# Kernel tuning notes

Measured on AMD Instinct MI355X. Metric: run time of the kernel, lower is better.

The kernel has to match this reference:

```python
import jax, jax.numpy as jnp
import numpy as np

NUM_CLASSES = 10
CLS_W, L1_W, GIOU_W = 2.0, 5.0, 2.0


def box_cxcywh_to_xyxy(b):
    cx, cy, w, h = b[..., 0], b[..., 1], b[..., 2], b[..., 3]
    return jnp.stack([cx - w / 2, cy - h / 2, cx + w / 2, cy + h / 2], axis=-1)


def giou_matrix(b1, b2):
    # b1: (B,N,4), b2: (B,M,4) xyxy -> (B,N,M)
    a1 = jnp.clip(b1[..., 2] - b1[..., 0], 0) * jnp.clip(b1[..., 3] - b1[..., 1], 0)
    a2 = jnp.clip(b2[..., 2] - b2[..., 0], 0) * jnp.clip(b2[..., 3] - b2[..., 1], 0)
    lt = jnp.maximum(b1[..., :, None, :2], b2[..., None, :, :2])
    rb = jnp.minimum(b1[..., :, None, 2:], b2[..., None, :, 2:])
    wh = jnp.clip(rb - lt, 0)
    inter = wh[..., 0] * wh[..., 1]
    union = a1[..., :, None] + a2[..., None, :] - inter
    iou = inter / jnp.clip(union, 1e-6)
    lte = jnp.minimum(b1[..., :, None, :2], b2[..., None, :, :2])
    rbe = jnp.maximum(b1[..., :, None, 2:], b2[..., None, :, 2:])
    whe = jnp.clip(rbe - lte, 0)
    enc = whe[..., 0] * whe[..., 1]
    return iou - (enc - union) / jnp.clip(enc, 1e-6)


def giou_elem(b1, b2):
    # b1, b2: (N,4) xyxy, paired -> (N,)
    a1 = jnp.clip(b1[:, 2] - b1[:, 0], 0) * jnp.clip(b1[:, 3] - b1[:, 1], 0)
    a2 = jnp.clip(b2[:, 2] - b2[:, 0], 0) * jnp.clip(b2[:, 3] - b2[:, 1], 0)
    lt = jnp.maximum(b1[:, :2], b2[:, :2])
    rb = jnp.minimum(b1[:, 2:], b2[:, 2:])
    wh = jnp.clip(rb - lt, 0)
    inter = wh[:, 0] * wh[:, 1]
    union = a1 + a2 - inter
    iou = inter / jnp.clip(union, 1e-6)
    lte = jnp.minimum(b1[:, :2], b2[:, :2])
    rbe = jnp.maximum(b1[:, 2:], b2[:, 2:])
    whe = jnp.clip(rbe - lte, 0)
    enc = whe[:, 0] * whe[:, 1]
    return iou - (enc - union) / jnp.clip(enc, 1e-6)


def hungarian(cost):
    # Jonker-Volgenant style shortest-augmenting-path assignment (== scipy.linear_sum_assignment)
    cost = np.asarray(cost, dtype=np.float64)
    transposed = cost.shape[0] > cost.shape[1]
    C = cost.T if transposed else cost
    n, m = C.shape  # n <= m
    u = np.zeros(n + 1)
    v = np.zeros(m + 1)
    p = np.zeros(m + 1, dtype=np.int64)
    colr = np.arange(m + 1)
    for i in range(1, n + 1):
        p[0] = i
        j0 = 0
        minv = np.full(m + 1, np.inf)
        way = np.zeros(m + 1, dtype=np.int64)
        used = np.zeros(m + 1, dtype=bool)
        while True:
            used[j0] = True
            i0 = p[j0]
            unused = colr[1:][~used[1:]]
            cur = C[i0 - 1, unused - 1] - u[i0] - v[unused]
            better = cur < minv[unused]
            bidx = unused[better]
            minv[bidx] = cur[better]
            way[bidx] = j0
            j1 = unused[np.argmin(minv[unused])]
            delta = minv[j1]
            u[p[used]] += delta
            v[used] -= delta
            minv[~used] -= delta
            j0 = j1
            if p[j0] == 0:
                break
        while j0 != 0:
            jn = way[j0]
            p[j0] = p[jn]
            j0 = jn
    rows = p[1:] - 1
    cols = np.arange(m)
    sel = rows >= 0
    r, c = rows[sel], cols[sel]
    if transposed:
        r, c = c, r
    order = np.argsort(r)
    return r[order], c[order]


def compute_matches(pred_logits, pred_boxes, gt_classes, gt_boxes):
    # Batched cost matrices on device, per-sample Hungarian on host (mirrors torch.no_grad matcher).
    B, Q, _ = pred_logits.shape
    G = gt_classes.shape[1]
    prob = jax.nn.softmax(pred_logits, axis=-1)
    cls_idx = jnp.clip(gt_classes, 0, NUM_CLASSES - 1)
    idx = jnp.broadcast_to(cls_idx[:, None, :], (B, Q, G))
    cls_cost = -jnp.take_along_axis(prob, idx, axis=2)                 # (B,Q,G)
    l1_cost = jnp.abs(pred_boxes[:, :, None, :] - gt_boxes[:, None, :, :]).sum(-1)
    g = giou_matrix(box_cxcywh_to_xyxy(pred_boxes), box_cxcywh_to_xyxy(gt_boxes))
    cost = CLS_W * cls_cost + L1_W * l1_cost - GIOU_W * g
    cost_np = np.asarray(jax.device_get(cost))
    valid_np = np.asarray(jax.device_get(gt_classes)) >= 0
    bs, ps, gs = [], [], []
    for bi in range(B):
        vidx = np.nonzero(valid_np[bi])[0]
        if vidx.size == 0:
            continue
        r, c = hungarian(cost_np[bi][:, vidx])
        bs.append(np.full(r.size, bi, dtype=np.int64))
        ps.append(r.astype(np.int64))
        gs.append(vidx[c].astype(np.int64))
    if bs:
        return np.concatenate(bs), np.concatenate(ps), np.concatenate(gs)
    z = np.zeros(0, np.int64)
    return z, z, z


def detection_loss(pred_logits, pred_boxes, gt_boxes, target_cls, b_f, p_f, g_f, n_matched):
    C1 = pred_logits.shape[-1]
    logp = jax.nn.log_softmax(pred_logits, axis=-1).reshape(-1, C1)
    t = target_cls.reshape(-1)
    w = jnp.ones(C1, dtype=pred_logits.dtype).at[-1].set(0.1)
    nll = -jnp.take_along_axis(logp, t[:, None], axis=1)[:, 0]
    wt = w[t]
    cls_loss = (wt * nll).sum() / wt.sum()
    mp = pred_boxes[b_f, p_f]
    mg = gt_boxes[b_f, g_f]
    l1 = jnp.abs(mp - mg).sum()
    gd = giou_elem(box_cxcywh_to_xyxy(mp), box_cxcywh_to_xyxy(mg))
    gl = (1.0 - gd).sum()
    return CLS_W * cls_loss + L1_W * l1 / n_matched + GIOU_W * gl / n_matched


def setup_inputs() -> dict:
    key = jax.random.key(0)
    k1, k2, k3, k4, k5 = jax.random.split(key, 5)
    B, Q, G, C = 64, 900, 100, NUM_CLASSES
    pred_logits = jax.random.normal(k1, (B, Q, C + 1), dtype=jnp.float32)
    pred_boxes = jax.random.uniform(k2, (B, Q, 4), dtype=jnp.float32, minval=0.05, maxval=0.6)
    gt_boxes = jax.random.uniform(k3, (B, G, 4), dtype=jnp.float32, minval=0.05, maxval=0.6)
    cls = jax.random.randint(k4, (B, G), 0, C)
    nvalid = jax.random.randint(k5, (B,), 1, G + 1)
    mask = jnp.arange(G)[None, :] < nvalid[:, None]
    gt_classes = jnp.where(mask, cls, -1).astype(jnp.int32)
    return {"pred_logits": pred_logits, "pred_boxes": pred_boxes,
            "gt_classes": gt_classes, "gt_boxes": gt_boxes}


def reference(pred_logits, pred_boxes, gt_classes, gt_boxes):
    B, Q = pred_logits.shape[:2]
    b_f, p_f, g_f = compute_matches(pred_logits, pred_boxes, gt_classes, gt_boxes)
    gt_np = np.asarray(jax.device_get(gt_classes))
    tc = np.full((B, Q), NUM_CLASSES, dtype=np.int32)
    tc[b_f, p_f] = gt_np[b_f, g_f]
    n_matched = max(int(b_f.size), 1)
    return detection_loss(pred_logits, pred_boxes, gt_boxes, jnp.asarray(tc), b_f, p_f, g_f, n_matched)
```

## Files before the change

### kernel.cpp

```cpp
#include <hip/hip_runtime.h>
#include <hip/hip_bf16.h>
#include <math.h>

#define BB 64
#define QQ 900
#define GG 100
#define NCLS 10
#define CP1 11

#define STRIDE 960
#define KPL 15
#define NT 512
#define NW 8
#define QMASK 255
#define ROUND_CAP 20000

#define NCH 8
#define QCH 128

#define CLS_W 2.0f
#define L1_W 5.0f
#define GIOU_W 2.0f

struct Accum {
  double wnll, wt, l1, gl;
  int nm, counter;
  int pad[6];
};

__global__ __launch_bounds__(256) void cost_kernel(
    const float* __restrict__ logits, const float* __restrict__ pboxes,
    const int* __restrict__ gcls, const float* __restrict__ gboxes,
    float* __restrict__ cost, float4* __restrict__ part, Accum* acc) {
  const int b = blockIdx.y;
  const int chunk = blockIdx.x;
  const int tid = threadIdx.x;
  const int ql = tid & (QCH - 1);
  const int gh = tid >> 7;
  const int q = chunk * QCH + ql;

  if (chunk == 0 && b == 0 && tid == 0) {
    acc->wnll = 0.0; acc->wt = 0.0; acc->l1 = 0.0; acc->gl = 0.0;
    acc->nm = 0; acc->counter = 0;
  }

  __shared__ float s_gb[GG * 4];
  __shared__ int   s_gc[GG];
  __shared__ float s_prob[QCH * 13];
  __shared__ float s_c[GG][QCH + 1];
  __shared__ float pm1[2][GG], pm2[2][GG];
  __shared__ int   pj1[2][GG];
  __shared__ int   sh_n;

  if (tid == 0) sh_n = 0;
  __syncthreads();

  for (int i = tid; i < GG * 4; i += 256) s_gb[i] = gboxes[b * GG * 4 + i];
  for (int i = tid; i < GG; i += 256) {
    const int v = gcls[b * GG + i];
    s_gc[i] = v;
    if (v >= 0) atomicAdd(&sh_n, 1);
  }

  float pcx = 0.f, pcy = 0.f, pw = 0.f, ph = 0.f;
  if (q < QQ) {
    const float* pb = pboxes + ((size_t)b * QQ + q) * 4;
    pcx = pb[0]; pcy = pb[1]; pw = pb[2]; ph = pb[3];
    if (gh == 0) {
      const float* lg = logits + ((size_t)b * QQ + q) * CP1;
      float l[CP1];
      float mx = -1e30f;
      for (int c = 0; c < CP1; ++c) { l[c] = lg[c]; mx = fmaxf(mx, l[c]); }
      float se = 0.f;
      for (int c = 0; c < CP1; ++c) { l[c] = expf(l[c] - mx); se += l[c]; }
      const float inv = 1.0f / se;
      for (int c = 0; c < NCLS; ++c) s_prob[ql * 13 + c] = l[c] * inv;
    }
  }
  __syncthreads();
  const int sn = sh_n;

  const float px1 = pcx - 0.5f * pw, py1 = pcy - 0.5f * ph;
  const float px2 = pcx + 0.5f * pw, py2 = pcy + 0.5f * ph;
  const float pa = fmaxf(px2 - px1, 0.f) * fmaxf(py2 - py1, 0.f);

  float* crow = cost + ((size_t)b * GG) * STRIDE + q;
  for (int g = gh; g < sn; g += 2) {
    float cv = 3e38f;
    if (q < QQ) {
      int cls = s_gc[g];
      cls = cls < 0 ? 0 : (cls > NCLS - 1 ? NCLS - 1 : cls);
      const float cc = -s_prob[ql * 13 + cls];
      const float gcx = s_gb[g * 4 + 0], gcy = s_gb[g * 4 + 1];
      const float gw  = s_gb[g * 4 + 2], gh2 = s_gb[g * 4 + 3];
      const float l1 = fabsf(pcx - gcx) + fabsf(pcy - gcy) + fabsf(pw - gw) + fabsf(ph - gh2);
      const float gx1 = gcx - 0.5f * gw, gy1 = gcy - 0.5f * gh2;
      const float gx2 = gcx + 0.5f * gw, gy2 = gcy + 0.5f * gh2;
      const float ga = fmaxf(gx2 - gx1, 0.f) * fmaxf(gy2 - gy1, 0.f);
      const float ltx = fmaxf(px1, gx1), lty = fmaxf(py1, gy1);
      const float rbx = fminf(px2, gx2), rby = fminf(py2, gy2);
      const float iw = fmaxf(rbx - ltx, 0.f), ih = fmaxf(rby - lty, 0.f);
      const float inter = iw * ih;
      const float uni = pa + ga - inter;
      const float iou = inter / fmaxf(uni, 1e-6f);
      const float ex1 = fminf(px1, gx1), ey1 = fminf(py1, gy1);
      const float ex2 = fmaxf(px2, gx2), ey2 = fmaxf(py2, gy2);
      const float ew = fmaxf(ex2 - ex1, 0.f), eh = fmaxf(ey2 - ey1, 0.f);
      const float enc = ew * eh;
      const float giou = iou - (enc - uni) / fmaxf(enc, 1e-6f);
      cv = CLS_W * cc + L1_W * l1 - GIOU_W * giou;
      crow[(size_t)g * STRIDE] = cv;
    } else if (q < STRIDE) {
      crow[(size_t)g * STRIDE] = 1e30f;
    }
    s_c[g][ql] = cv;
  }
  __syncthreads();

  {
    const int kmax = (chunk == NCH - 1) ? (QQ - (NCH - 1) * QCH) : QCH;
    const int half = tid >> 7;
    const int r = tid & 127;
    if (r < sn) {
      const int k0 = half ? 64 : 0;
      const int k1 = half ? kmax : (kmax < 64 ? kmax : 64);
      float m1 = 3e38f, m2 = 3e38f;
      int j1 = 0x7FFFFFFF;
      for (int k = k0; k < k1; ++k) {
        const float c = s_c[r][k];
        if (c < m1) { m2 = m1; m1 = c; j1 = 1 + chunk * QCH + k; }
        else if (c < m2) m2 = c;
      }
      pm1[half][r] = m1; pm2[half][r] = m2; pj1[half][r] = j1;
    }
    __syncthreads();
    if (tid < sn) {
      float m1 = pm1[0][tid], m2 = pm2[0][tid];
      int j1 = pj1[0][tid];
      const float n1 = pm1[1][tid], n2 = pm2[1][tid];
      const int i1 = pj1[1][tid];
      if (n1 < m1) { m2 = fminf(m1, n2); m1 = n1; j1 = i1; }
      else m2 = fminf(m2, n1);
      part[((size_t)b * NCH + chunk) * QCH + tid] = make_float4(m1, m2, __int_as_float(j1), 0.f);
    }
  }
}

__global__ __launch_bounds__(NT) void jv_kernel(
    const float* __restrict__ logits, const float* __restrict__ pboxes,
    const int* __restrict__ gcls, const float* __restrict__ gboxes,
    const float* __restrict__ cost, const float4* __restrict__ part,
    Accum* acc, float* out) {
  const int b = blockIdx.x;
  const int tid = threadIdx.x;
  const int lane = tid & 63;
  const int w = tid >> 6;

  __shared__ float vl[STRIDE + 2];
  __shared__ int   p[QQ + 1];
  __shared__ unsigned long long way64[STRIDE + 2];
  __shared__ float m1l[GG + 1], m2l[GG + 1];
  __shared__ int   aminl[GG + 1];
  __shared__ int   s_gc[GG];
  __shared__ int   queue[QMASK + 1];
  __shared__ int   sh_n, sh_qtail, sh_head;
  __shared__ double r0[NW], r1[NW], r2[NW], r3[NW];
  __shared__ int r4[NW];
  __shared__ float s_lse[QQ], s_mx[QQ];

  if (tid == 0) { sh_n = 0; sh_qtail = 0; sh_head = 0; }
  for (int j = tid; j <= QQ; j += NT) p[j] = 0;
  for (int j = tid; j < STRIDE + 2; j += NT) { vl[j] = 0.f; way64[j] = 0ull; }
  if (tid < GG) s_gc[tid] = gcls[b * GG + tid];
  __syncthreads();
  if (tid < GG && s_gc[tid] >= 0) atomicAdd(&sh_n, 1);
  __syncthreads();
  const int n = sh_n;
  const float* Cb = cost + (size_t)b * GG * STRIDE;

  for (int r = tid; r < n; r += NT) {
    float m1 = 3e38f, m2 = 3e38f;
    int j1 = 0x7FFFFFFF;
#pragma unroll
    for (int ch = 0; ch < NCH; ++ch) {
      const float4 pr = part[((size_t)b * NCH + ch) * QCH + r];
      const float pm1 = pr.x, pm2 = pr.y;
      if (pm1 < m1) { m2 = fminf(m1, pm2); m1 = pm1; j1 = __float_as_int(pr.z); }
      else m2 = fminf(m2, pm1);
    }
    m1l[r] = m1; m2l[r] = m2; aminl[r] = j1;
  }
  for (int qq = tid; qq < QQ; qq += NT) {
    const float* lg = logits + ((size_t)b * QQ + qq) * CP1;
    float l[CP1];
    float mx = -1e30f;
    for (int c = 0; c < CP1; ++c) { l[c] = lg[c]; mx = fmaxf(mx, l[c]); }
    float se = 0.f;
    for (int c = 0; c < CP1; ++c) se += expf(l[c] - mx);
    s_mx[qq] = mx;
    s_lse[qq] = logf(se);
  }
  __syncthreads();

  if (tid < n) {
    const float regret = m2l[tid] - m1l[tid];
    const unsigned long long key =
        ((unsigned long long)__float_as_uint(regret) << 20) | (unsigned long long)(tid + 1);
    atomicMax(&way64[aminl[tid]], key);
  }
  __syncthreads();
  if (tid < n) {
    const int j1 = aminl[tid];
    if ((int)(way64[j1] & 0xFFFFFu) == tid + 1) {
      p[j1] = tid + 1;
      vl[j1] = m1l[tid] - m2l[tid];
    } else {
      const int t0 = atomicAdd(&sh_qtail, 1);
      queue[t0 & QMASK] = tid + 1;
    }
  }
  __syncthreads();
  for (int j = tid; j < STRIDE + 2; j += NT) way64[j] = 0ull;
  __syncthreads();

  {
    float pfA[KPL], pfB[KPL];
    int pfAok = 0, pfBok = 0, pfArid = 0, pfBrid = 0;
    int kround = 0;
    while (kround < ROUND_CAP) {
      const int head = sh_head, tail = sh_qtail;
      const int nq = tail - head;
      if (nq <= 0) break;
      const int take = nq < 2 * NW ? nq : 2 * NW;
      ++kround;
      const bool doA = (2 * w < take);
      const bool doB = (2 * w + 1 < take);
      int ridA = 0, ridB = 0;
      float m1A = 3e38f, m2A = 3e38f, m1B = 3e38f, m2B = 3e38f;
      int j1A = 0x7FFFFFFF, j1B = 0x7FFFFFFF;
      if (doA) {
        float rcA[KPL], rcB[KPL];
        if (pfAok) { ridA = pfArid;
#pragma unroll
          for (int k = 0; k < KPL; ++k) rcA[k] = pfA[k];
        } else {
          ridA = queue[(head + 2 * w) & QMASK];
          const float* Cr = Cb + (size_t)(ridA - 1) * STRIDE + lane;
#pragma unroll
          for (int k = 0; k < KPL; ++k) rcA[k] = Cr[k << 6];
        }
        if (doB) {
          if (pfBok) { ridB = pfBrid;
#pragma unroll
            for (int k = 0; k < KPL; ++k) rcB[k] = pfB[k];
          } else {
            ridB = queue[(head + 2 * w + 1) & QMASK];
            const float* Cr = Cb + (size_t)(ridB - 1) * STRIDE + lane;
#pragma unroll
            for (int k = 0; k < KPL; ++k) rcB[k] = Cr[k << 6];
          }
        } else {
#pragma unroll
          for (int k = 0; k < KPL; ++k) rcB[k] = 3e38f;
        }
        float nA1 = 3e38f, nA2 = 3e38f, nB1 = 3e38f, nB2 = 3e38f;
        int iA1 = 0x7FFFFFFF, iB1 = 0x7FFFFFFF;
#pragma unroll
        for (int k = 0; k < 8; ++k) {
          const float vv = vl[1 + lane + (k << 6)];
          const float cA = rcA[k] - vv;
          if (cA < m1A) { m2A = m1A; m1A = cA; j1A = 1 + lane + (k << 6); }
          else if (cA < m2A) m2A = cA;
          const float cB = rcB[k] - vv;
          if (cB < m1B) { m2B = m1B; m1B = cB; j1B = 1 + lane + (k << 6); }
          else if (cB < m2B) m2B = cB;
        }
#pragma unroll
        for (int k = 8; k < KPL; ++k) {
          const float vv = vl[1 + lane + (k << 6)];
          const float cA = rcA[k] - vv;
          if (cA < nA1) { nA2 = nA1; nA1 = cA; iA1 = 1 + lane + (k << 6); }
          else if (cA < nA2) nA2 = cA;
          const float cB = rcB[k] - vv;
          if (cB < nB1) { nB2 = nB1; nB1 = cB; iB1 = 1 + lane + (k << 6); }
          else if (cB < nB2) nB2 = cB;
        }
        if (nA1 < m1A) { m2A = fminf(m1A, nA2); m1A = nA1; j1A = iA1; }
        else m2A = fminf(m2A, nA1);
        if (nB1 < m1B) { m2B = fminf(m1B, nB2); m1B = nB1; j1B = iB1; }
        else m2B = fminf(m2B, nB1);
        for (int m = 1; m < 64; m <<= 1) {
          const float oA1 = __shfl_xor(m1A, m), oA2 = __shfl_xor(m2A, m);
          const int ojA = __shfl_xor(j1A, m);
          const float oB1 = __shfl_xor(m1B, m), oB2 = __shfl_xor(m2B, m);
          const int ojB = __shfl_xor(j1B, m);
          if (oA1 < m1A) { m2A = fminf(m1A, oA2); m1A = oA1; j1A = ojA; }
          else m2A = fminf(m2A, oA1);
          if (oB1 < m1B) { m2B = fminf(m1B, oB2); m1B = oB1; j1B = ojB; }
          else m2B = fminf(m2B, oB1);
        }
        if (lane == 0) {
          float dA = m2A - m1A;
          if (dA < 0.f) dA = 0.f;
          const unsigned long long keyA = ((unsigned long long)kround << 44) |
              ((unsigned long long)__float_as_uint(dA) << 12) | (unsigned long long)ridA;
          atomicMax(&way64[j1A], keyA);
          if (doB) {
            float dB = m2B - m1B;
            if (dB < 0.f) dB = 0.f;
            const unsigned long long keyB = ((unsigned long long)kround << 44) |
                ((unsigned long long)__float_as_uint(dB) << 12) | (unsigned long long)ridB;
            atomicMax(&way64[j1B], keyB);
          }
        }
      }
      pfAok = 0; pfBok = 0;
      {
        const int nh = head + take;
        const int pA = nh + 2 * w, pB = pA + 1;
        if (pA < tail) {
          pfArid = queue[pA & QMASK];
          const float* Cr = Cb + (size_t)(pfArid - 1) * STRIDE + lane;
#pragma unroll
          for (int k = 0; k < KPL; ++k) pfA[k] = Cr[k << 6];
          pfAok = 1;
        }
        if (pB < tail) {
          pfBrid = queue[pB & QMASK];
          const float* Cr = Cb + (size_t)(pfBrid - 1) * STRIDE + lane;
#pragma unroll
          for (int k = 0; k < KPL; ++k) pfB[k] = Cr[k << 6];
          pfBok = 1;
        }
      }
      __syncthreads();
      if (lane == 0 && doA) {
        if ((int)(way64[j1A] & 0xFFFu) == ridA) {
          float dA = m2A - m1A;
          if (dA < 0.f) dA = 0.f;
          const float ov = vl[j1A];
          float nv = ov - dA;
          if (!(nv < ov)) nv = nextafterf(ov, -3e38f);
          vl[j1A] = nv;
          const int k0 = p[j1A];
          p[j1A] = ridA;
          if (k0 > 0) { const int t0 = atomicAdd(&sh_qtail, 1); queue[t0 & QMASK] = k0; }
        } else {
          const int t0 = atomicAdd(&sh_qtail, 1);
          queue[t0 & QMASK] = ridA;
        }
        if (doB) {
          if ((int)(way64[j1B] & 0xFFFu) == ridB) {
            float dB = m2B - m1B;
            if (dB < 0.f) dB = 0.f;
            const float ov = vl[j1B];
            float nv = ov - dB;
            if (!(nv < ov)) nv = nextafterf(ov, -3e38f);
            vl[j1B] = nv;
            const int k0 = p[j1B];
            p[j1B] = ridB;
            if (k0 > 0) { const int t0 = atomicAdd(&sh_qtail, 1); queue[t0 & QMASK] = k0; }
          } else {
            const int t0 = atomicAdd(&sh_qtail, 1);
            queue[t0 & QMASK] = ridB;
          }
        }
      }
      if (tid == 0) sh_head = head + take;
      __syncthreads();
    }
  }
  __syncthreads();

  double wnll = 0.0, wt = 0.0, l1d = 0.0, gld = 0.0;
  int nm = 0;
  for (int q = tid; q < QQ; q += NT) {
    const int idx = b * QQ + q;
    const int g = p[q + 1] - 1;
    const int t = (g >= 0) ? s_gc[g] : NCLS;
    const float lt = logits[(size_t)idx * CP1 + t];
    const float logp = (lt - s_mx[q]) - s_lse[q];
    const float wgt = (t == NCLS) ? 0.1f : 1.0f;
    wnll += (double)(wgt * (-logp));
    wt += (double)wgt;
    if (g >= 0) {
      nm += 1;
      const float* pb = pboxes + (size_t)idx * 4;
      const float* gb = gboxes + ((size_t)b * GG + g) * 4;
      const float pcx = pb[0], pcy = pb[1], pw = pb[2], ph = pb[3];
      const float gcx = gb[0], gcy = gb[1], gw = gb[2], gh = gb[3];
      const float l1 = fabsf(pcx - gcx) + fabsf(pcy - gcy) + fabsf(pw - gw) + fabsf(ph - gh);
      const float px1 = pcx - 0.5f * pw, py1 = pcy - 0.5f * ph;
      const float px2 = pcx + 0.5f * pw, py2 = pcy + 0.5f * ph;
      const float gx1 = gcx - 0.5f * gw, gy1 = gcy - 0.5f * gh;
      const float gx2 = gcx + 0.5f * gw, gy2 = gcy + 0.5f * gh;
      const float pa = fmaxf(px2 - px1, 0.f) * fmaxf(py2 - py1, 0.f);
      const float ga = fmaxf(gx2 - gx1, 0.f) * fmaxf(gy2 - gy1, 0.f);
      const float ltx = fmaxf(px1, gx1), lty = fmaxf(py1, gy1);
      const float rbx = fminf(px2, gx2), rby = fminf(py2, gy2);
      const float iw = fmaxf(rbx - ltx, 0.f), ih = fmaxf(rby - lty, 0.f);
      const float inter = iw * ih;
      const float uni = pa + ga - inter;
      const float iou = inter / fmaxf(uni, 1e-6f);
      const float ex1 = fminf(px1, gx1), ey1 = fminf(py1, gy1);
      const float ex2 = fmaxf(px2, gx2), ey2 = fmaxf(py2, gy2);
      const float ew = fmaxf(ex2 - ex1, 0.f), eh = fmaxf(ey2 - ey1, 0.f);
      const float enc = ew * eh;
      const float giou = iou - (enc - uni) / fmaxf(enc, 1e-6f);
      l1d += (double)l1;
      gld += (double)(1.0f - giou);
    }
  }

  for (int off = 32; off; off >>= 1) {
    wnll += __shfl_down(wnll, off);
    wt   += __shfl_down(wt, off);
    l1d  += __shfl_down(l1d, off);
    gld  += __shfl_down(gld, off);
    nm   += __shfl_down(nm, off);
  }
  if (lane == 0) { r0[w] = wnll; r1[w] = wt; r2[w] = l1d; r3[w] = gld; r4[w] = nm; }
  __syncthreads();
  if (tid == 0) {
    for (int x = 1; x < NW; ++x) { wnll += r0[x]; wt += r1[x]; l1d += r2[x]; gld += r3[x]; nm += r4[x]; }
    atomicAdd(&acc->wnll, wnll);
    atomicAdd(&acc->wt, wt);
    atomicAdd(&acc->l1, l1d);
    atomicAdd(&acc->gl, gld);
    atomicAdd(&acc->nm, nm);
    __threadfence();
    const int ticket = atomicAdd(&acc->counter, 1);
    if (ticket == BB - 1) {
      const double fw = atomicAdd(&acc->wnll, 0.0);
      const double fwt = atomicAdd(&acc->wt, 0.0);
      const double fl1 = atomicAdd(&acc->l1, 0.0);
      const double fgl = atomicAdd(&acc->gl, 0.0);
      int fnm = atomicAdd(&acc->nm, 0);
      if (fnm < 1) fnm = 1;
      const double loss = (double)CLS_W * (fw / fwt) +
                          ((double)L1_W * fl1 + (double)GIOU_W * fgl) / (double)fnm;
      out[0] = (float)loss;
    }
  }
}

extern "C" void kernel_launch(void* const* d_in, const int* in_sizes, int n_in,
                              void* d_out, int out_size, void* d_ws, size_t ws_size,
                              hipStream_t stream) {
  const float* logits = (const float*)d_in[0];
  const float* pboxes = (const float*)d_in[1];
  const int*   gcls   = (const int*)d_in[2];
  const float* gboxes = (const float*)d_in[3];

  char* ws = (char*)d_ws;
  Accum* acc = (Accum*)ws;
  float4* part = (float4*)(ws + 4096);
  float* cost = (float*)(ws + 4096 + (size_t)BB * NCH * QCH * sizeof(float4));

  cost_kernel<<<dim3(NCH, BB), 256, 0, stream>>>(logits, pboxes, gcls, gboxes, cost, part, acc);
  jv_kernel<<<BB, NT, 0, stream>>>(logits, pboxes, gcls, gboxes, cost, part, acc, (float*)d_out);
}
```

Measured before the change: 104.3 us.

## Split auction rounds by queue size and cache evicted rows' cost in LDS

The auction loop now has two paths. When at most one row per wave is queued, each wave handles a single row. It speculatively loads the cost row of the bidder it might evict and stores it in a per-wave LDS buffer tagged with the row id, so the next round can read that row from LDS instead of global memory. When more rows are queued, rows are assigned to waves with stride NW instead of interleaving, and prefetches are checked by queue position rather than a flag. This adds about 30 KB of LDS, which may lower occupancy, and adds extra global loads for speculative fetches that may go unused.

```diff
diff --git a/kernel.cpp b/kernel.cpp
--- a/kernel.cpp
+++ b/kernel.cpp
@@ -167,8 +167,11 @@
   __shared__ double r0[NW], r1[NW], r2[NW], r3[NW];
   __shared__ int r4[NW];
   __shared__ float s_lse[QQ], s_mx[QQ];
+  __shared__ float cbuf[NW][STRIDE];
+  __shared__ int   ctag[NW];
 
   if (tid == 0) { sh_n = 0; sh_qtail = 0; sh_head = 0; }
+  if (tid < NW) ctag[tid] = 0;
   for (int j = tid; j <= QQ; j += NT) p[j] = 0;
   for (int j = tid; j < STRIDE + 2; j += NT) { vl[j] = 0.f; way64[j] = 0ull; }
   if (tid < GG) s_gc[tid] = gcls[b * GG + tid];
@@ -225,7 +228,7 @@
 
   {
     float pfA[KPL], pfB[KPL];
-    int pfAok = 0, pfBok = 0, pfArid = 0, pfBrid = 0;
+    int pfApos = -1, pfBpos = -1, pfArid = 0, pfBrid = 0;
     int kround = 0;
     while (kround < ROUND_CAP) {
       const int head = sh_head, tail = sh_qtail;
@@ -233,141 +236,248 @@
       if (nq <= 0) break;
       const int take = nq < 2 * NW ? nq : 2 * NW;
       ++kround;
-      const bool doA = (2 * w < take);
-      const bool doB = (2 * w + 1 < take);
-      int ridA = 0, ridB = 0;
-      float m1A = 3e38f, m2A = 3e38f, m1B = 3e38f, m2B = 3e38f;
-      int j1A = 0x7FFFFFFF, j1B = 0x7FFFFFFF;
-      if (doA) {
-        float rcA[KPL], rcB[KPL];
-        if (pfAok) { ridA = pfArid;
-#pragma unroll
-          for (int k = 0; k < KPL; ++k) rcA[k] = pfA[k];
-        } else {
-          ridA = queue[(head + 2 * w) & QMASK];
-          const float* Cr = Cb + (size_t)(ridA - 1) * STRIDE + lane;
-#pragma unroll
-          for (int k = 0; k < KPL; ++k) rcA[k] = Cr[k << 6];
-        }
-        if (doB) {
-          if (pfBok) { ridB = pfBrid;
-#pragma unroll
-            for (int k = 0; k < KPL; ++k) rcB[k] = pfB[k];
+
+      if (take <= NW) {
+        const bool doA = (w < take);
+        int ridA = 0;
+        float m1A = 3e38f, m2A = 3e38f;
+        int j1A = 0x7FFFFFFF;
+        int k0A = 0;
+        float sfA[KPL];
+        if (doA) {
+          const int posA = head + w;
+          float rcA[KPL];
+          if (pfApos == posA) {
+            ridA = pfArid;
+#pragma unroll
+            for (int k = 0; k < KPL; ++k) rcA[k] = pfA[k];
           } else {
-            ridB = queue[(head + 2 * w + 1) & QMASK];
-            const float* Cr = Cb + (size_t)(ridB - 1) * STRIDE + lane;
-#pragma unroll
-            for (int k = 0; k < KPL; ++k) rcB[k] = Cr[k << 6];
-          }
-        } else {
-#pragma unroll
-          for (int k = 0; k < KPL; ++k) rcB[k] = 3e38f;
-        }
-        float nA1 = 3e38f, nA2 = 3e38f, nB1 = 3e38f, nB2 = 3e38f;
-        int iA1 = 0x7FFFFFFF, iB1 = 0x7FFFFFFF;
-#pragma unroll
-        for (int k = 0; k < 8; ++k) {
-          const float vv = vl[1 + lane + (k << 6)];
-          const float cA = rcA[k] - vv;
-          if (cA < m1A) { m2A = m1A; m1A = cA; j1A = 1 + lane + (k << 6); }
-          else if (cA < m2A) m2A = cA;
-          const float cB = rcB[k] - vv;
-          if (cB < m1B) { m2B = m1B; m1B = cB; j1B = 1 + lane + (k << 6); }
-          else if (cB < m2B) m2B = cB;
-        }
-#pragma unroll
-        for (int k = 8; k < KPL; ++k) {
-          const float vv = vl[1 + lane + (k << 6)];
-          const float cA = rcA[k] - vv;
-          if (cA < nA1) { nA2 = nA1; nA1 = cA; iA1 = 1 + lane + (k << 6); }
-          else if (cA < nA2) nA2 = cA;
-          const float cB = rcB[k] - vv;
-          if (cB < nB1) { nB2 = nB1; nB1 = cB; iB1 = 1 + lane + (k << 6); }
-          else if (cB < nB2) nB2 = cB;
-        }
-        if (nA1 < m1A) { m2A = fminf(m1A, nA2); m1A = nA1; j1A = iA1; }
-        else m2A = fminf(m2A, nA1);
-        if (nB1 < m1B) { m2B = fminf(m1B, nB2); m1B = nB1; j1B = iB1; }
-        else m2B = fminf(m2B, nB1);
-        for (int m = 1; m < 64; m <<= 1) {
-          const float oA1 = __shfl_xor(m1A, m), oA2 = __shfl_xor(m2A, m);
-          const int ojA = __shfl_xor(j1A, m);
-          const float oB1 = __shfl_xor(m1B, m), oB2 = __shfl_xor(m2B, m);
-          const int ojB = __shfl_xor(j1B, m);
-          if (oA1 < m1A) { m2A = fminf(m1A, oA2); m1A = oA1; j1A = ojA; }
-          else m2A = fminf(m2A, oA1);
-          if (oB1 < m1B) { m2B = fminf(m1B, oB2); m1B = oB1; j1B = ojB; }
-          else m2B = fminf(m2B, oB1);
-        }
-        if (lane == 0) {
-          float dA = m2A - m1A;
-          if (dA < 0.f) dA = 0.f;
-          const unsigned long long keyA = ((unsigned long long)kround << 44) |
-              ((unsigned long long)__float_as_uint(dA) << 12) | (unsigned long long)ridA;
-          atomicMax(&way64[j1A], keyA);
-          if (doB) {
-            float dB = m2B - m1B;
-            if (dB < 0.f) dB = 0.f;
-            const unsigned long long keyB = ((unsigned long long)kround << 44) |
-                ((unsigned long long)__float_as_uint(dB) << 12) | (unsigned long long)ridB;
-            atomicMax(&way64[j1B], keyB);
-          }
-        }
-      }
-      pfAok = 0; pfBok = 0;
-      {
-        const int nh = head + take;
-        const int pA = nh + 2 * w, pB = pA + 1;
-        if (pA < tail) {
-          pfArid = queue[pA & QMASK];
-          const float* Cr = Cb + (size_t)(pfArid - 1) * STRIDE + lane;
-#pragma unroll
-          for (int k = 0; k < KPL; ++k) pfA[k] = Cr[k << 6];
-          pfAok = 1;
-        }
-        if (pB < tail) {
-          pfBrid = queue[pB & QMASK];
-          const float* Cr = Cb + (size_t)(pfBrid - 1) * STRIDE + lane;
-#pragma unroll
-          for (int k = 0; k < KPL; ++k) pfB[k] = Cr[k << 6];
-          pfBok = 1;
-        }
-      }
-      __syncthreads();
-      if (lane == 0 && doA) {
-        if ((int)(way64[j1A] & 0xFFFu) == ridA) {
-          float dA = m2A - m1A;
-          if (dA < 0.f) dA = 0.f;
-          const float ov = vl[j1A];
-          float nv = ov - dA;
-          if (!(nv < ov)) nv = nextafterf(ov, -3e38f);
-          vl[j1A] = nv;
-          const int k0 = p[j1A];
-          p[j1A] = ridA;
-          if (k0 > 0) { const int t0 = atomicAdd(&sh_qtail, 1); queue[t0 & QMASK] = k0; }
-        } else {
-          const int t0 = atomicAdd(&sh_qtail, 1);
-          queue[t0 & QMASK] = ridA;
-        }
-        if (doB) {
-          if ((int)(way64[j1B] & 0xFFFu) == ridB) {
-            float dB = m2B - m1B;
-            if (dB < 0.f) dB = 0.f;
-            const float ov = vl[j1B];
-            float nv = ov - dB;
+            ridA = queue[posA & QMASK];
+            const unsigned long long hit =
+                __ballot((lane < NW) && (ctag[lane] == ridA));
+            if (hit) {
+              const int slot = __ffsll((long long)hit) - 1;
+#pragma unroll
+              for (int k = 0; k < KPL; ++k) rcA[k] = cbuf[slot][lane + (k << 6)];
+            } else {
+              const float* Cr = Cb + (size_t)(ridA - 1) * STRIDE + lane;
+#pragma unroll
+              for (int k = 0; k < KPL; ++k) rcA[k] = Cr[k << 6];
+            }
+          }
+          float nA1 = 3e38f, nA2 = 3e38f;
+          int iA1 = 0x7FFFFFFF;
+#pragma unroll
+          for (int k = 0; k < 8; ++k) {
+            const float cA = rcA[k] - vl[1 + lane + (k << 6)];
+            if (cA < m1A) { m2A = m1A; m1A = cA; j1A = 1 + lane + (k << 6); }
+            else if (cA < m2A) m2A = cA;
+          }
+#pragma unroll
+          for (int k = 8; k < KPL; ++k) {
+            const float cA = rcA[k] - vl[1 + lane + (k << 6)];
+            if (cA < nA1) { nA2 = nA1; nA1 = cA; iA1 = 1 + lane + (k << 6); }
+            else if (cA < nA2) nA2 = cA;
+          }
+          if (nA1 < m1A) { m2A = fminf(m1A, nA2); m1A = nA1; j1A = iA1; }
+          else m2A = fminf(m2A, nA1);
+          for (int m = 1; m < 64; m <<= 1) {
+            const float oA1 = __shfl_xor(m1A, m), oA2 = __shfl_xor(m2A, m);
+            const int ojA = __shfl_xor(j1A, m);
+            if (oA1 < m1A) { m2A = fminf(m1A, oA2); m1A = oA1; j1A = ojA; }
+            else m2A = fminf(m2A, oA1);
+          }
+          k0A = p[j1A];
+          if (k0A > 0) {
+            const float* Cr = Cb + (size_t)(k0A - 1) * STRIDE + lane;
+#pragma unroll
+            for (int k = 0; k < KPL; ++k) sfA[k] = Cr[k << 6];
+          }
+          if (lane == 0) {
+            float dA = m2A - m1A;
+            if (dA < 0.f) dA = 0.f;
+            const unsigned long long keyA = ((unsigned long long)kround << 44) |
+                ((unsigned long long)__float_as_uint(dA) << 12) | (unsigned long long)ridA;
+            atomicMax(&way64[j1A], keyA);
+          }
+        }
+        pfApos = -1; pfBpos = -1;
+        {
+          const int nh = head + take;
+          const int pA = nh + w;
+          if (pA < tail) {
+            pfArid = queue[pA & QMASK];
+            const float* Cr = Cb + (size_t)(pfArid - 1) * STRIDE + lane;
+#pragma unroll
+            for (int k = 0; k < KPL; ++k) pfA[k] = Cr[k << 6];
+            pfApos = pA;
+          }
+        }
+        __syncthreads();
+        if (doA && k0A > 0) {
+#pragma unroll
+          for (int k = 0; k < KPL; ++k) cbuf[w][lane + (k << 6)] = sfA[k];
+          if (lane == 0) ctag[w] = k0A;
+        }
+        if (lane == 0 && doA) {
+          if ((int)(way64[j1A] & 0xFFFu) == ridA) {
+            float dA = m2A - m1A;
+            if (dA < 0.f) dA = 0.f;
+            const float ov = vl[j1A];
+            float nv = ov - dA;
             if (!(nv < ov)) nv = nextafterf(ov, -3e38f);
-            vl[j1B] = nv;
-            const int k0 = p[j1B];
-            p[j1B] = ridB;
+            vl[j1A] = nv;
+            const int k0 = p[j1A];
+            p[j1A] = ridA;
             if (k0 > 0) { const int t0 = atomicAdd(&sh_qtail, 1); queue[t0 & QMASK] = k0; }
           } else {
             const int t0 = atomicAdd(&sh_qtail, 1);
-            queue[t0 & QMASK] = ridB;
-          }
-        }
+            queue[t0 & QMASK] = ridA;
+          }
+        }
+        if (tid == 0) sh_head = head + take;
+        __syncthreads();
+      } else {
+        const bool doA = (w < take);
+        const bool doB = (NW + w < take);
+        int ridA = 0, ridB = 0;
+        float m1A = 3e38f, m2A = 3e38f, m1B = 3e38f, m2B = 3e38f;
+        int j1A = 0x7FFFFFFF, j1B = 0x7FFFFFFF;
+        {
+          float rcA[KPL], rcB[KPL];
+          const int posA = head + w;
+          if (pfApos == posA) {
+            ridA = pfArid;
+#pragma unroll
+            for (int k = 0; k < KPL; ++k) rcA[k] = pfA[k];
+          } else {
+            ridA = queue[posA & QMASK];
+            const float* Cr = Cb + (size_t)(ridA - 1) * STRIDE + lane;
+#pragma unroll
+            for (int k = 0; k < KPL; ++k) rcA[k] = Cr[k << 6];
+          }
+          if (doB) {
+            const int posB = head + NW + w;
+            if (pfBpos == posB) {
+              ridB = pfBrid;
+#pragma unroll
+              for (int k = 0; k < KPL; ++k) rcB[k] = pfB[k];
+            } else {
+              ridB = queue[posB & QMASK];
+              const float* Cr = Cb + (size_t)(ridB - 1) * STRIDE + lane;
+#pragma unroll
+              for (int k = 0; k < KPL; ++k) rcB[k] = Cr[k << 6];
+            }
+          } else {
+#pragma unroll
+            for (int k = 0; k < KPL; ++k) rcB[k] = 3e38f;
+          }
+          float nA1 = 3e38f, nA2 = 3e38f, nB1 = 3e38f, nB2 = 3e38f;
+          int iA1 = 0x7FFFFFFF, iB1 = 0x7FFFFFFF;
+#pragma unroll
+          for (int k = 0; k < 8; ++k) {
+            const float vv = vl[1 + lane + (k << 6)];
+            const float cA = rcA[k] - vv;
+            if (cA < m1A) { m2A = m1A; m1A = cA; j1A = 1 + lane + (k << 6); }
+            else if (cA < m2A) m2A = cA;
+            const float cB = rcB[k] - vv;
+            if (cB < m1B) { m2B = m1B; m1B = cB; j1B = 1 + lane + (k << 6); }
+            else if (cB < m2B) m2B = cB;
+          }
+#pragma unroll
+          for (int k = 8; k < KPL; ++k) {
+            const float vv = vl[1 + lane + (k << 6)];
+            const float cA = rcA[k] - vv;
+            if (cA < nA1) { nA2 = nA1; nA1 = cA; iA1 = 1 + lane + (k << 6); }
+            else if (cA < nA2) nA2 = cA;
+            const float cB = rcB[k] - vv;
+            if (cB < nB1) { nB2 = nB1; nB1 = cB; iB1 = 1 + lane + (k << 6); }
+            else if (cB < nB2) nB2 = cB;
+          }
+          if (nA1 < m1A) { m2A = fminf(m1A, nA2); m1A = nA1; j1A = iA1; }
+          else m2A = fminf(m2A, nA1);
+          if (nB1 < m1B) { m2B = fminf(m1B, nB2); m1B = nB1; j1B = iB1; }
+          else m2B = fminf(m2B, nB1);
+          for (int m = 1; m < 64; m <<= 1) {
+            const float oA1 = __shfl_xor(m1A, m), oA2 = __shfl_xor(m2A, m);
+            const int ojA = __shfl_xor(j1A, m);
+            const float oB1 = __shfl_xor(m1B, m), oB2 = __shfl_xor(m2B, m);
+            const int ojB = __shfl_xor(j1B, m);
+            if (oA1 < m1A) { m2A = fminf(m1A, oA2); m1A = oA1; j1A = ojA; }
+            else m2A = fminf(m2A, oA1);
+            if (oB1 < m1B) { m2B = fminf(m1B, oB2); m1B = oB1; j1B = ojB; }
+            else m2B = fminf(m2B, oB1);
+          }
+          if (lane == 0) {
+            float dA = m2A - m1A;
+            if (dA < 0.f) dA = 0.f;
+            const unsigned long long keyA = ((unsigned long long)kround << 44) |
+                ((unsigned long long)__float_as_uint(dA) << 12) | (unsigned long long)ridA;
+            atomicMax(&way64[j1A], keyA);
+            if (doB) {
+              float dB = m2B - m1B;
+              if (dB < 0.f) dB = 0.f;
+              const unsigned long long keyB = ((unsigned long long)kround << 44) |
+                  ((unsigned long long)__float_as_uint(dB) << 12) | (unsigned long long)ridB;
+              atomicMax(&way64[j1B], keyB);
+            }
+          }
+        }
+        pfApos = -1; pfBpos = -1;
+        {
+          const int nh = head + take;
+          const int pA = nh + w, pB = nh + NW + w;
+          if (pA < tail) {
+            pfArid = queue[pA & QMASK];
+            const float* Cr = Cb + (size_t)(pfArid - 1) * STRIDE + lane;
+#pragma unroll
+            for (int k = 0; k < KPL; ++k) pfA[k] = Cr[k << 6];
+            pfApos = pA;
+          }
+          if (pB < tail) {
+            pfBrid = queue[pB & QMASK];
+            const float* Cr = Cb + (size_t)(pfBrid - 1) * STRIDE + lane;
+#pragma unroll
+            for (int k = 0; k < KPL; ++k) pfB[k] = Cr[k << 6];
+            pfBpos = pB;
+          }
+        }
+        __syncthreads();
+        if (lane == 0 && doA) {
+          if ((int)(way64[j1A] & 0xFFFu) == ridA) {
+            float dA = m2A - m1A;
+            if (dA < 0.f) dA = 0.f;
+            const float ov = vl[j1A];
+            float nv = ov - dA;
+            if (!(nv < ov)) nv = nextafterf(ov, -3e38f);
+            vl[j1A] = nv;
+            const int k0 = p[j1A];
+            p[j1A] = ridA;
+            if (k0 > 0) { const int t0 = atomicAdd(&sh_qtail, 1); queue[t0 & QMASK] = k0; }
+          } else {
+            const int t0 = atomicAdd(&sh_qtail, 1);
+            queue[t0 & QMASK] = ridA;
+          }
+          if (doB) {
+            if ((int)(way64[j1B] & 0xFFFu) == ridB) {
+              float dB = m2B - m1B;
+              if (dB < 0.f) dB = 0.f;
+              const float ov = vl[j1B];
+              float nv = ov - dB;
+              if (!(nv < ov)) nv = nextafterf(ov, -3e38f);
+              vl[j1B] = nv;
+              const int k0 = p[j1B];
+              p[j1B] = ridB;
+              if (k0 > 0) { const int t0 = atomicAdd(&sh_qtail, 1); queue[t0 & QMASK] = k0; }
+            } else {
+              const int t0 = atomicAdd(&sh_qtail, 1);
+              queue[t0 & QMASK] = ridB;
+            }
+          }
+        }
+        if (tid == 0) sh_head = head + take;
+        __syncthreads();
       }
-      if (tid == 0) sh_head = head + take;
-      __syncthreads();
     }
   }
   __syncthreads();
```

Result: no change. 102.8 us (-1.4%).
